# Kernel tuning notes

Hardware: AMD Instinct MI355X
Metric: run time of the kernel (lower is better)

The kernel has to match this reference:

```python
import jax, jax.numpy as jnp
import numpy as np

N_POINTS = 524288
N_VOXELS = 32768
C_IN = 6
GF = 64          # gf_dim
C_OUT = 256      # output_channels
HALF = C_OUT // 2


def _linear_params(key, fin, fout):
    kw, kb = jax.random.split(key)
    bound = 1.0 / np.sqrt(fin)
    W = jax.random.uniform(kw, (fin, fout), jnp.float32, -bound, bound)
    b = jax.random.uniform(kb, (fout,), jnp.float32, -bound, bound)
    return W, b


def setup_inputs() -> dict:
    key = jax.random.key(0)
    ks = jax.random.split(key, 8)
    inp_feat = jax.random.normal(ks[0], (N_POINTS, C_IN), dtype=jnp.float32)
    vox2point_idx = jax.random.randint(ks[1], (N_POINTS,), 0, N_VOXELS, dtype=jnp.int64)
    W1, b1 = _linear_params(ks[2], C_IN, GF)          # point_lin1
    W2, b2 = _linear_params(ks[3], GF, HALF)          # point_lin2
    Wv1, bv1 = _linear_params(ks[4], HALF, HALF)      # vox_lin1
    W3, b3 = _linear_params(ks[5], C_OUT, C_OUT)      # point_lin3
    W4, b4 = _linear_params(ks[6], C_OUT, C_OUT)      # point_lin4
    Wv2, bv2 = _linear_params(ks[7], C_OUT, C_OUT)    # vox_lin2
    return {
        "inp_feat": inp_feat, "vox2point_idx": vox2point_idx, "num_voxels": N_VOXELS,
        "W1": W1, "b1": b1, "W2": W2, "b2": b2, "Wv1": Wv1, "bv1": bv1,
        "W3": W3, "b3": b3, "W4": W4, "b4": b4, "Wv2": Wv2, "bv2": bv2,
    }


def reference(inp_feat, vox2point_idx, num_voxels,
              W1, b1, W2, b2, Wv1, bv1, W3, b3, W4, b4, Wv2, bv2):
    relu = jax.nn.relu
    # per-point MLP: [N,6] -> [N,64] -> [N,128]
    point_feat1 = relu(inp_feat @ W1 + b1)
    point_feat2 = relu(point_feat1 @ W2 + b2)
    # scatter-max pooling over voxels: [N,128] -> [V,128]
    occ_voxel_feat = jax.ops.segment_max(point_feat2, vox2point_idx,
                                         num_segments=num_voxels)
    occ_voxel_feat = relu(occ_voxel_feat @ Wv1 + bv1)
    # gather voxel feature back to points and concat: [N,128]+[N,128] -> [N,256]
    point_global_feat = occ_voxel_feat[vox2point_idx]
    point_feat3 = jnp.concatenate((point_global_feat, point_feat2), axis=-1)
    point_feat4 = relu(point_feat3 @ W3 + b3)
    point_feat5 = relu(point_feat4 @ W4 + b4)
    # second scatter-max pooling: [N,256] -> [V,256]
    occ_voxel_feat2 = jax.ops.segment_max(point_feat5, vox2point_idx,
                                          num_segments=num_voxels)
    occ_voxel_feat2 = relu(occ_voxel_feat2 @ Wv2 + bv2)
    return occ_voxel_feat2
```

## Files before the change

### kernel.cpp

```cpp
#include <hip/hip_runtime.h>


#define NPTS 524288
#define NVOX 32768

typedef _Float16 f16;
typedef _Float16 f16x4 __attribute__((ext_vector_type(4)));
typedef _Float16 f16x8 __attribute__((ext_vector_type(8)));
typedef float f32x4 __attribute__((ext_vector_type(4)));

#define GLDS16(g, l)                                                          \
  __builtin_amdgcn_global_load_lds(                                           \
      (const __attribute__((address_space(1))) unsigned int*)(const void*)(g),\
      (__attribute__((address_space(3))) unsigned int*)(void*)(l), 16, 0, 0)

__global__ void k_fixidx(const int* __restrict__ raw, int* __restrict__ out) {
  bool is64 = true;
#pragma unroll
  for (int k = 0; k < 32; ++k)
    if (raw[2 * k + 1] != 0) is64 = false;
  int stride = gridDim.x * blockDim.x;
  for (int i = blockIdx.x * blockDim.x + threadIdx.x; i < NPTS; i += stride)
    out[i] = is64 ? raw[2 * i] : raw[i];
}

__global__ void k_hist(const int* __restrict__ idx, int* __restrict__ counts) {
  int stride = gridDim.x * blockDim.x;
  for (int i = blockIdx.x * blockDim.x + threadIdx.x; i < NPTS; i += stride)
    atomicAdd(&counts[idx[i]], 1);
}

__global__ void k_scan(const int* __restrict__ counts, int* __restrict__ offsets) {
  __shared__ int part[1024];
  __shared__ int sums[32];
  int t = threadIdx.x;
  int loc[32];
  int s = 0;
#pragma unroll
  for (int j = 0; j < 32; ++j) { loc[j] = counts[t * 32 + j]; s += loc[j]; }
  part[t] = s;
  __syncthreads();
  if (t < 32) {
    int run = 0;
    for (int j = 0; j < 32; ++j) { int tmp = part[t * 32 + j]; part[t * 32 + j] = run; run += tmp; }
    sums[t] = run;
  }
  __syncthreads();
  if (t == 0) {
    int run = 0;
    for (int i = 0; i < 32; ++i) { int tmp = sums[i]; sums[i] = run; run += tmp; }
  }
  __syncthreads();
  int b = part[t] + sums[t >> 5];
#pragma unroll
  for (int j = 0; j < 32; ++j) { offsets[t * 32 + j] = b; b += loc[j]; }
  if (t == 1023) offsets[NVOX] = b;
}

__global__ void k_scat(const int* __restrict__ idx, const int* __restrict__ offsets,
                       int* __restrict__ cursor, int* __restrict__ sp, int* __restrict__ sv) {
  int stride = gridDim.x * blockDim.x;
  for (int i = blockIdx.x * blockDim.x + threadIdx.x; i < NPTS; i += stride) {
    int v = idx[i];
    int pos = offsets[v] + atomicAdd(&cursor[v], 1);
    sp[pos] = i;
    sv[pos] = v;
  }
}

__global__ void k_mlp1(const float* __restrict__ x, const int* __restrict__ sp,
                       const float* __restrict__ W1, const float* __restrict__ b1,
                       f16* __restrict__ pf1) {
  __shared__ float w[384];
  __shared__ float bb[64];
  int t = threadIdx.x;
  if (t < 384) w[t] = W1[t];
  if (t < 64) bb[t] = b1[t];
  __syncthreads();
  int stride = gridDim.x * blockDim.x;
  for (int s = blockIdx.x * blockDim.x + t; s < NPTS; s += stride) {
    int p = sp[s];
    const float* src = x + (size_t)p * 6;
    float x0 = src[0], x1 = src[1], x2 = src[2];
    float x3 = src[3], x4 = src[4], x5 = src[5];
    f16* dst = pf1 + (size_t)s * 64;
#pragma unroll
    for (int j0 = 0; j0 < 64; j0 += 8) {
      f16x8 o;
#pragma unroll
      for (int u = 0; u < 8; ++u) {
        int j = j0 + u;
        float a = bb[j];
        a += x0 * w[j];       a += x1 * w[64 + j];
        a += x2 * w[128 + j]; a += x3 * w[192 + j];
        a += x4 * w[256 + j]; a += x5 * w[320 + j];
        o[u] = (f16)fmaxf(a, 0.f);
      }
      *(f16x8*)(dst + j0) = o;
    }
  }
}

__global__ void k_wcast(const float* __restrict__ W, f16* __restrict__ Wt, int K, int N) {
  int g = blockIdx.x * blockDim.x + threadIdx.x;
  if (g >= K * N) return;
  int k = g / N, n = g % N;
  Wt[n * K + k] = (f16)W[g];
}

__global__ void k_castf(const float* __restrict__ in, f16* __restrict__ out, int n) {
  int stride = gridDim.x * blockDim.x;
  for (int i = blockIdx.x * blockDim.x + threadIdx.x; i < n; i += stride)
    out[i] = (f16)in[i];
}

template <int K, int N, int MODEA, bool SCATTER, bool OUTF32, bool WRITEO, bool WTILE>
__global__ __launch_bounds__(256, 3) void k_gemm(
    const f16* __restrict__ A,
    const int* __restrict__ sv, const int* __restrict__ sp,
    const int* __restrict__ offs,
    const float* __restrict__ x, const float* __restrict__ W1, const float* __restrict__ b1,
    const f16* __restrict__ Bt,
    const float* __restrict__ bias,
    f16* __restrict__ Of16, float* __restrict__ Of32, int row0) {
  constexpr int NT = N / 128;
  __shared__ __align__(16) char smem[32768];
  __shared__ float xs[MODEA == 2 ? 768 : 1];
  __shared__ int svp[MODEA == 2 ? 128 : 1];
  __shared__ int svx[SCATTER ? 128 : 1];
  f16* As = (f16*)smem;
  f16* Bs = As + 128 * 64;

  int nwg = gridDim.x;
  int bid = blockIdx.x;
  int q = nwg >> 3;
  int swz = (bid & 7) * q + (bid >> 3);
  int tm = swz / NT, tn = swz % NT;
  int t = threadIdx.x;

  if (MODEA == 2) { if (t < 128) svp[t] = sp[row0 + tm * 128 + t]; }
  if (SCATTER) { if (t < 128) svx[t] = sv[row0 + tm * 128 + t]; }
  if (MODEA == 2) __syncthreads();

  int l = t & 63, w = t >> 6;
  int wm = w >> 1, wn = w & 1;
  int lrow = l & 15, lk = l >> 4;
  f32x4 acc[4][4] = {};

  constexpr int KT = K / 64;
#pragma unroll
  for (int kt = 0; kt < KT; ++kt) {
    int k0 = kt * 64;
#pragma unroll
    for (int i = 0; i < 4; ++i) {
      int n = i * 32 + (t >> 3);
      int clog = (t & 7) ^ (n & 7);
      GLDS16(Bt + (size_t)(tn * 128 + n) * K + k0 + clog * 8, Bs + i * 2048 + t * 8);
    }
    if constexpr (MODEA == 2) {
      for (int g = t; g < 768; g += 256) xs[g] = x[(size_t)svp[g / 6] * 6 + (g % 6)];
      __syncthreads();
      int j = t & 63;
      float wv[6];
#pragma unroll
      for (int i = 0; i < 6; ++i) wv[i] = W1[i * 64 + j];
      float bb = b1[j];
      int rb = (t >> 6) * 32;
#pragma unroll
      for (int rr = 0; rr < 32; ++rr) {
        int row = rb + rr;
        float a = bb;
#pragma unroll
        for (int i = 0; i < 6; ++i) a += xs[row * 6 + i] * wv[i];
        As[row * 64 + (((j >> 3) ^ (row & 7)) << 3) + (j & 7)] = (f16)fmaxf(a, 0.f);
      }
    } else {
#pragma unroll
      for (int i = 0; i < 4; ++i) {
        int row = i * 32 + (t >> 3);
        int clog = (t & 7) ^ (row & 7);
        GLDS16(A + (size_t)(tm * 128 + row) * K + k0 + clog * 8, As + i * 2048 + t * 8);
      }
    }
    __syncthreads();
#pragma unroll
    for (int ks = 0; ks < 2; ++ks) {
      f16x8 af[4], bf[4];
#pragma unroll
      for (int m = 0; m < 4; ++m) {
        int row = wm * 64 + m * 16 + lrow;
        int cp = (ks * 4 + lk) ^ (row & 7);
        af[m] = *(const f16x8*)(As + row * 64 + cp * 8);
      }
#pragma unroll
      for (int n = 0; n < 4; ++n) {
        int col = wn * 64 + n * 16 + lrow;
        int cp = (ks * 4 + lk) ^ (col & 7);
        bf[n] = *(const f16x8*)(Bs + col * 64 + cp * 8);
      }
#pragma unroll
      for (int m = 0; m < 4; ++m)
#pragma unroll
        for (int n = 0; n < 4; ++n)
          acc[m][n] = __builtin_amdgcn_mfma_f32_16x16x32_f16(af[m], bf[n], acc[m][n], 0, 0, 0);
    }
    __syncthreads();
  }

  if constexpr (WRITEO) {
#pragma unroll
    for (int m = 0; m < 4; ++m)
#pragma unroll
      for (int n = 0; n < 4; ++n)
#pragma unroll
        for (int j = 0; j < 4; ++j) {
          int row = wm * 64 + m * 16 + lk * 4 + j;
          int gc  = tn * 128 + wn * 64 + n * 16 + lrow;
          float val = fmaxf(acc[m][n][j] + bias[gc], 0.f);
          if constexpr (OUTF32) Of32[(size_t)(tm * 128 + row) * N + gc] = val;
          else                  Of16[(size_t)(tm * 128 + row) * N + gc] = (f16)val;
        }
  }

  if constexpr (SCATTER) {
    f16* tile = (f16*)smem;
#pragma unroll
    for (int m = 0; m < 4; ++m)
#pragma unroll
      for (int n = 0; n < 4; ++n)
#pragma unroll
        for (int j = 0; j < 4; ++j) {
          int row = wm * 64 + m * 16 + lk * 4 + j;
          int col = wn * 64 + n * 16 + lrow;
          tile[row * 128 + col] =
              (f16)fmaxf(acc[m][n][j] + bias[tn * 128 + col], 0.f);
        }
    __syncthreads();
    if constexpr (WTILE) {
      f16* dst = Of16 + (size_t)(row0 + tm * 128) * 128;
#pragma unroll
      for (int i = 0; i < 8; ++i) {
        int g = i * 256 + t;
        *(f16x8*)(dst + g * 8) = *(const f16x8*)(tile + g * 8);
      }
    }
    int c = t & 127, h = t >> 7;
    int r0l = h * 64;
    int gc = tn * 128 + c;
    int grow0 = row0 + tm * 128 + r0l;
    float run = 0.f;
    int curv = svx[r0l];
    for (int r = r0l; r < r0l + 64; ++r) {
      int v = svx[r];
      if (v != curv) {
        bool inter = (offs[curv] >= grow0) && (offs[curv + 1] <= grow0 + 64);
        if (inter) Of32[(size_t)curv * N + gc] = run;
        else atomicMax((int*)&Of32[(size_t)curv * N + gc], __float_as_int(run));
        curv = v; run = 0.f;
      }
      run = fmaxf(run, (float)tile[r * 128 + c]);
    }
    bool inter = (offs[curv] >= grow0) && (offs[curv + 1] <= grow0 + 64);
    if (inter) Of32[(size_t)curv * N + gc] = run;
    else atomicMax((int*)&Of32[(size_t)curv * N + gc], __float_as_int(run));
  }
}

__global__ __launch_bounds__(512, 2) void k_stage2(
    const f16* __restrict__ pf2, const f16* __restrict__ occ1,
    const int* __restrict__ sv, const int* __restrict__ offs,
    const f16* __restrict__ W3t, const float* __restrict__ b3,
    const f16* __restrict__ W4t, const float* __restrict__ b4,
    float* __restrict__ vox2f, int row0) {
  __shared__ __align__(16) f16 Bs[256 * 32];
  __shared__ __align__(16) f16 PF[64 * 288];
  __shared__ int svx[64];

  int nwg = gridDim.x;
  int bid = blockIdx.x;
  int q = nwg >> 3;
  int bm = (bid & 7) * q + (bid >> 3);
  int t = threadIdx.x;
  int l = t & 63, w = t >> 6;
  int lrow = l & 15, lk = l >> 4;

  if (t < 64) svx[t] = sv[row0 + bm * 64 + t];
  __syncthreads();

  f16* Afull = PF;
#pragma unroll
  for (int ii = 0; ii < 4; ++ii) {
    int g = ii * 512 + t;
    int row = g >> 5, cs = g & 31;
    int cl = (cs & 24) | ((cs ^ row) & 7);
    const f16* src;
    if (cl < 16) src = occ1 + (size_t)svx[row] * 128 + cl * 8;
    else         src = pf2 + (size_t)(bm * 64 + row) * 128 + (cl - 16) * 8;
    GLDS16(src, Afull + g * 8);
  }
#pragma unroll
  for (int ii = 0; ii < 2; ++ii) {
    int g = ii * 512 + t;
    int n = g >> 2, c = g & 3;
    int cl = c ^ ((n >> 1) & 3);
    GLDS16(W3t + (size_t)n * 256 + cl * 8, Bs + g * 8);
  }
  __syncthreads();

  f32x4 acc[4][2] = {};

#pragma unroll
  for (int p = 0; p < 8; ++p) {
    f16x8 bf[2];
#pragma unroll
    for (int n = 0; n < 2; ++n) {
      int col = w * 32 + n * 16 + lrow;
      int cp = lk ^ ((col >> 1) & 3);
      bf[n] = *(const f16x8*)(Bs + col * 32 + cp * 8);
    }
    __syncthreads();
    {
      const f16* Wsrc = (p < 7) ? W3t : W4t;
      int kc = (p < 7) ? (p + 1) : 0;
#pragma unroll
      for (int ii = 0; ii < 2; ++ii) {
        int g = ii * 512 + t;
        int n = g >> 2, c = g & 3;
        int cl = c ^ ((n >> 1) & 3);
        GLDS16(Wsrc + (size_t)n * 256 + kc * 32 + cl * 8, Bs + g * 8);
      }
    }
    __builtin_amdgcn_s_setprio(1);
    f16x8 af[4];
#pragma unroll
    for (int m = 0; m < 4; ++m) {
      int row = m * 16 + lrow;
      int ab = p * 4 + lk;
      int slot = (ab & 24) | ((ab ^ row) & 7);
      af[m] = *(const f16x8*)(Afull + row * 256 + slot * 8);
    }
#pragma unroll
    for (int m = 0; m < 4; ++m)
#pragma unroll
      for (int n = 0; n < 2; ++n)
        acc[m][n] = __builtin_amdgcn_mfma_f32_16x16x32_f16(af[m], bf[n], acc[m][n], 0, 0, 0);
    __builtin_amdgcn_s_setprio(0);
    __syncthreads();
  }

  f16* pf4 = PF;
#pragma unroll
  for (int m = 0; m < 4; ++m)
#pragma unroll
    for (int n = 0; n < 2; ++n)
#pragma unroll
      for (int j = 0; j < 4; ++j) {
        int row  = m * 16 + lk * 4 + j;
        int colg = w * 32 + n * 16 + lrow;
        pf4[row * 264 + colg] = (f16)fmaxf(acc[m][n][j] + b3[colg], 0.f);
      }
  __syncthreads();

#pragma unroll
  for (int m = 0; m < 4; ++m)
#pragma unroll
    for (int n = 0; n < 2; ++n)
      acc[m][n] = (f32x4){0.f, 0.f, 0.f, 0.f};

#pragma unroll
  for (int p = 0; p < 8; ++p) {
    f16x8 bf[2];
#pragma unroll
    for (int n = 0; n < 2; ++n) {
      int col = w * 32 + n * 16 + lrow;
      int cp = lk ^ ((col >> 1) & 3);
      bf[n] = *(const f16x8*)(Bs + col * 32 + cp * 8);
    }
    __syncthreads();
    if (p < 7) {
#pragma unroll
      for (int ii = 0; ii < 2; ++ii) {
        int g = ii * 512 + t;
        int n = g >> 2, c = g & 3;
        int cl = c ^ ((n >> 1) & 3);
        GLDS16(W4t + (size_t)n * 256 + (p + 1) * 32 + cl * 8, Bs + g * 8);
      }
    }
    __builtin_amdgcn_s_setprio(1);
    f16x8 af[4];
#pragma unroll
    for (int m = 0; m < 4; ++m) {
      int row = m * 16 + lrow;
      int chunk = p * 4 + lk;
      af[m] = *(const f16x8*)(pf4 + row * 264 + chunk * 8);
    }
#pragma unroll
    for (int m = 0; m < 4; ++m)
#pragma unroll
      for (int n = 0; n < 2; ++n)
        acc[m][n] = __builtin_amdgcn_mfma_f32_16x16x32_f16(af[m], bf[n], acc[m][n], 0, 0, 0);
    __builtin_amdgcn_s_setprio(0);
    __syncthreads();
  }

  f16* pf5 = PF;
#pragma unroll
  for (int m = 0; m < 4; ++m)
#pragma unroll
    for (int n = 0; n < 2; ++n) {
      int colg = w * 32 + n * 16 + lrow;
      int rowb = m * 16 + lk * 4;
      float bv = b4[colg];
      f16x4 v;
#pragma unroll
      for (int j = 0; j < 4; ++j) v[j] = (f16)fmaxf(acc[m][n][j] + bv, 0.f);
      *(f16x4*)(pf5 + colg * 72 + rowb) = v;
    }
  __syncthreads();

  {
    int c = t & 255, seg = t >> 8;
    int r0l = seg * 32;
    int grow0 = row0 + bm * 64 + r0l;
    const f16* colp = pf5 + c * 72;
    float run = 0.f;
    int curv = svx[r0l];
#pragma unroll
    for (int rb = 0; rb < 32; rb += 8) {
      f16x8 vv = *(const f16x8*)(colp + r0l + rb);
#pragma unroll
      for (int u = 0; u < 8; ++u) {
        int r = r0l + rb + u;
        int v = svx[r];
        if (v != curv) {
          bool inter = (offs[curv] >= grow0) && (offs[curv + 1] <= grow0 + 32);
          if (inter) vox2f[(size_t)curv * 256 + c] = run;
          else atomicMax((int*)&vox2f[(size_t)curv * 256 + c], __float_as_int(run));
          curv = v; run = 0.f;
        }
        run = fmaxf(run, (float)vv[u]);
      }
    }
    bool inter = (offs[curv] >= grow0) && (offs[curv + 1] <= grow0 + 32);
    if (inter) vox2f[(size_t)curv * 256 + c] = run;
    else atomicMax((int*)&vox2f[(size_t)curv * 256 + c], __float_as_int(run));
  }
}

extern "C" void kernel_launch(void* const* d_in, const int* in_sizes, int n_in,
                              void* d_out, int out_size, void* d_ws, size_t ws_size,
                              hipStream_t stream) {
  const float* x   = (const float*)d_in[0];
  const int*  idxr = (const int*)d_in[1];
  const float* W1  = (const float*)d_in[3];
  const float* b1  = (const float*)d_in[4];
  const float* W2  = (const float*)d_in[5];
  const float* b2  = (const float*)d_in[6];
  const float* Wv1 = (const float*)d_in[7];
  const float* bv1 = (const float*)d_in[8];
  const float* W3  = (const float*)d_in[9];
  const float* b3  = (const float*)d_in[10];
  const float* W4  = (const float*)d_in[11];
  const float* b4  = (const float*)d_in[12];
  const float* Wv2 = (const float*)d_in[13];
  const float* bv2 = (const float*)d_in[14];
  float* out = (float*)d_out;

  char* ws = (char*)d_ws;
  size_t off = 0;
  auto alloc = [&](size_t bytes) {
    void* p = ws + off;
    off = (off + bytes + 255) & ~(size_t)255;
    return p;
  };
  int* idx     = (int*)alloc((size_t)NPTS * 4);
  int* counts  = (int*)alloc((size_t)NVOX * 4);
  int* cursor  = (int*)alloc((size_t)NVOX * 4);
  int* offs    = (int*)alloc((size_t)(NVOX + 1) * 4);
  int* sp      = (int*)alloc((size_t)NPTS * 4);
  int* sv      = (int*)alloc((size_t)NPTS * 4);
  f16* W2t     = (f16*)alloc(64 * 128 * 2);
  f16* Wv1t    = (f16*)alloc(128 * 128 * 2);
  f16* W3t     = (f16*)alloc(256 * 256 * 2);
  f16* W4t     = (f16*)alloc(256 * 256 * 2);
  f16* Wv2t    = (f16*)alloc(256 * 256 * 2);
  float* vox1f = (float*)alloc((size_t)NVOX * 128 * 4);
  f16* vox1h   = (f16*)alloc((size_t)NVOX * 128 * 2);
  f16* occ1    = (f16*)alloc((size_t)NVOX * 128 * 2);
  float* vox2f = (float*)alloc((size_t)NVOX * 256 * 4);

  size_t rem = (ws_size > off) ? ws_size - off : 0;
  bool PF2FULL = rem >= (size_t)NPTS * 256 + 4096;
  int CH = 65536;
  f16* pf2   = (f16*)alloc(PF2FULL ? (size_t)NPTS * 256 : (size_t)CH * 256);
  f16* vox2h = pf2;
  size_t rem2 = (ws_size > off) ? ws_size - off : 0;
  bool MLP1SPLIT = PF2FULL && rem2 >= (size_t)NPTS * 128 + 4096;
  f16* pf1 = MLP1SPLIT ? (f16*)alloc((size_t)NPTS * 128) : nullptr;

  hipMemsetAsync(counts, 0, (size_t)NVOX * 4, stream);
  hipMemsetAsync(cursor, 0, (size_t)NVOX * 4, stream);
  hipMemsetAsync(vox1f, 0, (size_t)NVOX * 128 * 4, stream);
  hipMemsetAsync(vox2f, 0, (size_t)NVOX * 256 * 4, stream);

  k_fixidx<<<2048, 256, 0, stream>>>(idxr, idx);
  k_wcast<<<(64 * 128 + 255) / 256, 256, 0, stream>>>(W2, W2t, 64, 128);
  k_wcast<<<(128 * 128 + 255) / 256, 256, 0, stream>>>(Wv1, Wv1t, 128, 128);
  k_wcast<<<(256 * 256 + 255) / 256, 256, 0, stream>>>(W3, W3t, 256, 256);
  k_wcast<<<(256 * 256 + 255) / 256, 256, 0, stream>>>(W4, W4t, 256, 256);
  k_wcast<<<(256 * 256 + 255) / 256, 256, 0, stream>>>(Wv2, Wv2t, 256, 256);
  k_hist<<<2048, 256, 0, stream>>>(idx, counts);
  k_scan<<<1, 1024, 0, stream>>>(counts, offs);
  k_scat<<<2048, 256, 0, stream>>>(idx, offs, cursor, sp, sv);

  if (MLP1SPLIT) {
    k_mlp1<<<2048, 256, 0, stream>>>(x, sp, W1, b1, pf1);
    k_gemm<64, 128, 0, true, false, false, true><<<NPTS / 128, 256, 0, stream>>>(
        pf1, sv, sp, offs, x, W1, b1, W2t, b2, pf2, vox1f, 0);
  } else if (PF2FULL) {
    k_gemm<64, 128, 2, true, false, false, true><<<NPTS / 128, 256, 0, stream>>>(
        nullptr, sv, sp, offs, x, W1, b1, W2t, b2, pf2, vox1f, 0);
  } else {
    k_gemm<64, 128, 2, true, false, false, false><<<NPTS / 128, 256, 0, stream>>>(
        nullptr, sv, sp, offs, x, W1, b1, W2t, b2, nullptr, vox1f, 0);
  }
  k_castf<<<2048, 256, 0, stream>>>(vox1f, vox1h, NVOX * 128);
  k_gemm<128, 128, 0, false, false, true, false><<<NVOX / 128, 256, 0, stream>>>(
      vox1h, nullptr, nullptr, nullptr, nullptr, nullptr, nullptr,
      Wv1t, bv1, occ1, nullptr, 0);

  if (PF2FULL) {
    k_stage2<<<NPTS / 64, 512, 0, stream>>>(
        pf2, occ1, sv, offs, W3t, b3, W4t, b4, vox2f, 0);
  } else {
    for (int c = 0; c < NPTS / CH; ++c) {
      int row0 = c * CH;
      k_gemm<64, 128, 2, false, false, true, false><<<CH / 128, 256, 0, stream>>>(
          nullptr, nullptr, sp, nullptr, x, W1, b1, W2t, b2, pf2, nullptr, row0);
      k_stage2<<<CH / 64, 512, 0, stream>>>(
          pf2, occ1, sv, offs, W3t, b3, W4t, b4, vox2f, row0);
    }
  }

  k_castf<<<2048, 256, 0, stream>>>(vox2f, vox2h, NVOX * 256);
  k_gemm<256, 256, 0, false, true, true, false><<<(NVOX / 128) * 2, 256, 0, stream>>>(
      vox2h, nullptr, nullptr, nullptr, nullptr, nullptr, nullptr,
      Wv2t, bv2, nullptr, out, 0);
}
```

Before: 381.1 us.

## Load stage2 weight fragments directly from global instead of LDS staging

In k_stage2, W3/W4 B-fragments are no longer staged through a shared-memory buffer with per-step barriers. Each lane now reads its f16x8 weight fragment straight from global memory, relying on cache since the weights are shared by all workgroups. This removes the Bs array, which shrinks LDS use, and drops the per-k-step __syncthreads. The loops are also marked unroll 1. The trade-off is that weight loads now sit on the MFMA critical path as global-load latency with no prefetch.

```diff
diff --git a/kernel.cpp b/kernel.cpp
--- a/kernel.cpp
+++ b/kernel.cpp
@@ -272,7 +272,6 @@
     const f16* __restrict__ W3t, const float* __restrict__ b3,
     const f16* __restrict__ W4t, const float* __restrict__ b4,
     float* __restrict__ vox2f, int row0) {
-  __shared__ __align__(16) f16 Bs[256 * 32];
   __shared__ __align__(16) f16 PF[64 * 288];
   __shared__ int svx[64];
 
@@ -298,38 +297,18 @@
     else         src = pf2 + (size_t)(bm * 64 + row) * 128 + (cl - 16) * 8;
     GLDS16(src, Afull + g * 8);
   }
-#pragma unroll
-  for (int ii = 0; ii < 2; ++ii) {
-    int g = ii * 512 + t;
-    int n = g >> 2, c = g & 3;
-    int cl = c ^ ((n >> 1) & 3);
-    GLDS16(W3t + (size_t)n * 256 + cl * 8, Bs + g * 8);
-  }
   __syncthreads();
 
   f32x4 acc[4][2] = {};
-
-#pragma unroll
+  const f16* w3c0 = W3t + (size_t)(w * 32 + lrow) * 256 + lk * 8;
+  const f16* w3c1 = w3c0 + 16 * 256;
+  const f16* w4c0 = W4t + (size_t)(w * 32 + lrow) * 256 + lk * 8;
+  const f16* w4c1 = w4c0 + 16 * 256;
+
+#pragma unroll 1
   for (int p = 0; p < 8; ++p) {
-    f16x8 bf[2];
-#pragma unroll
-    for (int n = 0; n < 2; ++n) {
-      int col = w * 32 + n * 16 + lrow;
-      int cp = lk ^ ((col >> 1) & 3);
-      bf[n] = *(const f16x8*)(Bs + col * 32 + cp * 8);
-    }
-    __syncthreads();
-    {
-      const f16* Wsrc = (p < 7) ? W3t : W4t;
-      int kc = (p < 7) ? (p + 1) : 0;
-#pragma unroll
-      for (int ii = 0; ii < 2; ++ii) {
-        int g = ii * 512 + t;
-        int n = g >> 2, c = g & 3;
-        int cl = c ^ ((n >> 1) & 3);
-        GLDS16(Wsrc + (size_t)n * 256 + kc * 32 + cl * 8, Bs + g * 8);
-      }
-    }
+    f16x8 bf0 = *(const f16x8*)(w3c0 + p * 32);
+    f16x8 bf1 = *(const f16x8*)(w3c1 + p * 32);
     __builtin_amdgcn_s_setprio(1);
     f16x8 af[4];
 #pragma unroll
@@ -340,13 +319,13 @@
       af[m] = *(const f16x8*)(Afull + row * 256 + slot * 8);
     }
 #pragma unroll
-    for (int m = 0; m < 4; ++m)
-#pragma unroll
-      for (int n = 0; n < 2; ++n)
-        acc[m][n] = __builtin_amdgcn_mfma_f32_16x16x32_f16(af[m], bf[n], acc[m][n], 0, 0, 0);
+    for (int m = 0; m < 4; ++m) {
+      acc[m][0] = __builtin_amdgcn_mfma_f32_16x16x32_f16(af[m], bf0, acc[m][0], 0, 0, 0);
+      acc[m][1] = __builtin_amdgcn_mfma_f32_16x16x32_f16(af[m], bf1, acc[m][1], 0, 0, 0);
+    }
     __builtin_amdgcn_s_setprio(0);
-    __syncthreads();
-  }
+  }
+  __syncthreads();
 
   f16* pf4 = PF;
 #pragma unroll
@@ -367,25 +346,10 @@
     for (int n = 0; n < 2; ++n)
       acc[m][n] = (f32x4){0.f, 0.f, 0.f, 0.f};
 
-#pragma unroll
+#pragma unroll 1
   for (int p = 0; p < 8; ++p) {
-    f16x8 bf[2];
-#pragma unroll
-    for (int n = 0; n < 2; ++n) {
-      int col = w * 32 + n * 16 + lrow;
-      int cp = lk ^ ((col >> 1) & 3);
-      bf[n] = *(const f16x8*)(Bs + col * 32 + cp * 8);
-    }
-    __syncthreads();
-    if (p < 7) {
-#pragma unroll
-      for (int ii = 0; ii < 2; ++ii) {
-        int g = ii * 512 + t;
-        int n = g >> 2, c = g & 3;
-        int cl = c ^ ((n >> 1) & 3);
-        GLDS16(W4t + (size_t)n * 256 + (p + 1) * 32 + cl * 8, Bs + g * 8);
-      }
-    }
+    f16x8 bf0 = *(const f16x8*)(w4c0 + p * 32);
+    f16x8 bf1 = *(const f16x8*)(w4c1 + p * 32);
     __builtin_amdgcn_s_setprio(1);
     f16x8 af[4];
 #pragma unroll
@@ -395,13 +359,13 @@
       af[m] = *(const f16x8*)(pf4 + row * 264 + chunk * 8);
     }
 #pragma unroll
-    for (int m = 0; m < 4; ++m)
-#pragma unroll
-      for (int n = 0; n < 2; ++n)
-        acc[m][n] = __builtin_amdgcn_mfma_f32_16x16x32_f16(af[m], bf[n], acc[m][n], 0, 0, 0);
+    for (int m = 0; m < 4; ++m) {
+      acc[m][0] = __builtin_amdgcn_mfma_f32_16x16x32_f16(af[m], bf0, acc[m][0], 0, 0, 0);
+      acc[m][1] = __builtin_amdgcn_mfma_f32_16x16x32_f16(af[m], bf1, acc[m][1], 0, 0, 0);
+    }
     __builtin_amdgcn_s_setprio(0);
-    __syncthreads();
-  }
+  }
+  __syncthreads();
 
   f16* pf5 = PF;
 #pragma unroll
```

Result: slower. 447.4 us (+17.4%).
